# Kernel optimization log

Hardware: AMD Instinct MI355X
Metric: run time of the kernel (lower is better)

Reference implementation:

```python
import jax, jax.numpy as jnp
import numpy as np

TEMPERATURE = 0.1
WEIGHT = 0.1
EPS = 1e-12  # F.normalize clamp_min eps

B = 512   # number of reactions (batches)
G = 128   # atoms per reaction per side (uniform groups)
D = 256   # feature dim


def setup_inputs() -> dict:
    key = jax.random.key(0)
    k1, k2, k3, k4 = jax.random.split(key, 4)
    preds = jax.random.normal(k1, (B,), dtype=jnp.float32)
    y = jax.random.normal(k2, (B,), dtype=jnp.float32)
    reactant_features = jax.random.normal(k3, (B * G, D), dtype=jnp.float32)
    product_features = jax.random.normal(k4, (B * G, D), dtype=jnp.float32)
    # sorted, uniform-size groups: [0]*G, [1]*G, ...
    batch_idx = jnp.repeat(jnp.arange(B, dtype=jnp.int64), G)
    return {
        "preds": preds,
        "y": y,
        "reactant_features": reactant_features,
        "product_features": product_features,
        "reactant_batch_indices": batch_idx,
        "product_batch_indices": batch_idx,
    }


def _l2_normalize(x):
    # matches F.normalize(p=2, dim=1): x / max(||x||, eps)
    n = jnp.sqrt(jnp.sum(x * x, axis=-1, keepdims=True))
    return x / jnp.maximum(n, EPS)


def reference(preds, y, reactant_features, product_features,
              reactant_batch_indices, product_batch_indices):
    # MSE with reduction='sum'
    mse_loss = jnp.sum((preds - y) ** 2)

    # groups are uniform and sorted -> per-batch gather == reshape
    nb = int(reactant_batch_indices[-1]) + 1          # number of unique batches
    g = reactant_features.shape[0] // nb
    d = reactant_features.shape[1]
    r = reactant_features.reshape(nb, g, d)
    p = product_features.reshape(nb, g, d)

    rn = _l2_normalize(r)
    pn = _l2_normalize(p)
    # per-batch similarity [nb, g, g]
    sim = jnp.einsum('bgd,bhd->bgh', rn, pn) / TEMPERATURE

    # cross_entropy with labels = arange(g), mean over rows (torch default)
    lse = jax.scipy.special.logsumexp(sim, axis=-1)   # [nb, g]
    diag = jnp.einsum('bgg->bg', sim)                 # logits at true labels
    ce_per_batch = jnp.mean(lse - diag, axis=-1)      # [nb]
    contrastive_loss = jnp.mean(ce_per_batch)         # sum over batches / nb

    return mse_loss + WEIGHT * contrastive_loss
```

## Files before the change

kernel.cpp:

```cpp
#include <hip/hip_runtime.h>
#include <math.h>

#define BATCH 512
#define G 128
#define D 256
#define LRB 264

typedef __attribute__((ext_vector_type(8))) short short8;
typedef __attribute__((ext_vector_type(4))) float f32x4;
typedef __attribute__((ext_vector_type(4))) int  i32x4;

__device__ __forceinline__ unsigned int pack2bf16(float a, float b) {
    unsigned int ua = __float_as_uint(a);
    unsigned int ub = __float_as_uint(b);
    ua = (ua + 0x7FFFu + ((ua >> 16) & 1u)) >> 16;
    ub = (ub + 0x7FFFu + ((ub >> 16) & 1u)) >> 16;
    return ua | (ub << 16);
}

#define WAITVM(N)  asm volatile("s_waitcnt vmcnt(" #N ")" ::: "memory")
#define WAITLGKM0  asm volatile("s_waitcnt lgkmcnt(0)" ::: "memory")
#define FENCE      asm volatile("" ::: "memory")

__global__ __launch_bounds__(512, 4)
void fused_kernel(const float* __restrict__ rfeat,
                  const float* __restrict__ pfeat,
                  const float* __restrict__ preds,
                  const float* __restrict__ yv,
                  float* __restrict__ out)
{
    const int b = blockIdx.x;
    const float* rb = rfeat + (size_t)b * (G * D);
    const float* pb = pfeat + (size_t)b * (G * D);

    __shared__ unsigned short psh[G * LRB];
    __shared__ float inv_r[G];
    __shared__ float inv_p[G];
    __shared__ float red[8];

    const int tid  = threadIdx.x;
    const int lane = tid & 63;
    const int wv   = tid >> 6;
    const int lg   = lane >> 4;
    const int lc   = lane & 15;
    const int prow = tid >> 3;
    const int psl  = tid & 7;

    float pd = 0.f, yd = 0.f;
    if (b == 0) { pd = preds[tid]; yd = yv[tid]; }
    FENCE;

    float4 pv[8];
#pragma unroll
    for (int j = 0; j < 8; ++j)
        pv[j] = *reinterpret_cast<const float4*>(pb + prow * D + (psl + 8 * j) * 4);
    FENCE;

    const float* rptr = rb + (wv * 16 + lc) * D + lg * 8;
    float4 rx[16];
#pragma unroll
    for (int ks = 0; ks < 8; ++ks) {
        rx[2 * ks]     = *reinterpret_cast<const float4*>(rptr + ks * 32);
        rx[2 * ks + 1] = *reinterpret_cast<const float4*>(rptr + ks * 32 + 4);
    }
    FENCE;

    WAITVM(16);
    float contrib = 0.f;
    if (b == 0) { float dd = pd - yd; contrib = dd * dd; }
    {
        float ss = 0.f;
#pragma unroll
        for (int j = 0; j < 8; ++j) {
            const float4 v = pv[j];
            ss += v.x*v.x + v.y*v.y + v.z*v.z + v.w*v.w;
            *reinterpret_cast<uint2*>(&psh[prow * LRB + (psl + 8 * j) * 4]) =
                make_uint2(pack2bf16(v.x, v.y), pack2bf16(v.z, v.w));
        }
#pragma unroll
        for (int off = 1; off < 8; off <<= 1) ss += __shfl_xor(ss, off);
        if (psl == 0) inv_p[prow] = 1.0f / fmaxf(sqrtf(ss), 1e-12f);
    }
    FENCE;

#pragma unroll
    for (int j = 0; j < 8; ++j)
        pv[j] = *reinterpret_cast<const float4*>(pb + (64 + prow) * D + (psl + 8 * j) * 4);
    FENCE;

    WAITVM(8);
    short8 afr[8];
    float nrsum = 0.f;
#pragma unroll
    for (int ks = 0; ks < 8; ++ks) {
        const float4 x0 = rx[2 * ks], x1 = rx[2 * ks + 1];
        nrsum += x0.x*x0.x + x0.y*x0.y + x0.z*x0.z + x0.w*x0.w
               + x1.x*x1.x + x1.y*x1.y + x1.z*x1.z + x1.w*x1.w;
        i32x4 pk = { (int)pack2bf16(x0.x, x0.y), (int)pack2bf16(x0.z, x0.w),
                     (int)pack2bf16(x1.x, x1.y), (int)pack2bf16(x1.z, x1.w) };
        union { i32x4 i; short8 s; } u; u.i = pk;
        afr[ks] = u.s;
    }
    nrsum += __shfl_xor(nrsum, 16);
    nrsum += __shfl_xor(nrsum, 32);
    if (lane < 16)
        inv_r[wv * 16 + lane] = 10.0f / fmaxf(sqrtf(nrsum), 1e-12f);

    WAITLGKM0;
    __builtin_amdgcn_s_barrier();
    FENCE;

    f32x4 acc[8];
#pragma unroll
    for (int nj = 0; nj < 8; ++nj) acc[nj] = (f32x4){0.f, 0.f, 0.f, 0.f};

#pragma unroll
    for (int ks = 0; ks < 8; ++ks) {
        const int kb = ks * 32 + lg * 8;
#pragma unroll
        for (int nj = 0; nj < 4; ++nj) {
            short8 bf = *reinterpret_cast<const short8*>(&psh[(nj * 16 + lc) * LRB + kb]);
            acc[nj] = __builtin_amdgcn_mfma_f32_16x16x32_bf16(afr[ks], bf, acc[nj], 0, 0, 0);
        }
    }
    FENCE;

    WAITVM(0);
    {
        float ss = 0.f;
#pragma unroll
        for (int j = 0; j < 8; ++j) {
            const float4 v = pv[j];
            ss += v.x*v.x + v.y*v.y + v.z*v.z + v.w*v.w;
            *reinterpret_cast<uint2*>(&psh[(64 + prow) * LRB + (psl + 8 * j) * 4]) =
                make_uint2(pack2bf16(v.x, v.y), pack2bf16(v.z, v.w));
        }
#pragma unroll
        for (int off = 1; off < 8; off <<= 1) ss += __shfl_xor(ss, off);
        if (psl == 0) inv_p[64 + prow] = 1.0f / fmaxf(sqrtf(ss), 1e-12f);
    }

    WAITLGKM0;
    __builtin_amdgcn_s_barrier();
    FENCE;

#pragma unroll
    for (int ks = 0; ks < 8; ++ks) {
        const int kb = ks * 32 + lg * 8;
#pragma unroll
        for (int nj = 4; nj < 8; ++nj) {
            short8 bf = *reinterpret_cast<const short8*>(&psh[(nj * 16 + lc) * LRB + kb]);
            acc[nj] = __builtin_amdgcn_mfma_f32_16x16x32_bf16(afr[ks], bf, acc[nj], 0, 0, 0);
        }
    }

    float invp_r[8];
#pragma unroll
    for (int nj = 0; nj < 8; ++nj) invp_r[nj] = inv_p[nj * 16 + lc];

    const int njd = wv;
    float ce_part = 0.f;
#pragma unroll
    for (int reg = 0; reg < 4; ++reg) {
        const int rrow = lg * 4 + reg;
        const float invr_g = inv_r[wv * 16 + rrow];
        float s[8];
        float m = -3.0e38f;
#pragma unroll
        for (int nj = 0; nj < 8; ++nj) {
            s[nj] = acc[nj][reg] * invr_g * invp_r[nj];
            m = fmaxf(m, s[nj]);
        }
#pragma unroll
        for (int off = 1; off < 16; off <<= 1) m = fmaxf(m, __shfl_xor(m, off));
        float e = 0.f;
#pragma unroll
        for (int nj = 0; nj < 8; ++nj) e += __expf(s[nj] - m);
#pragma unroll
        for (int off = 1; off < 16; off <<= 1) e += __shfl_xor(e, off);
        if (lc == rrow)
            ce_part += (m + __logf(e)) - s[njd];
    }

    contrib += ce_part * (0.1f / ((float)BATCH * (float)G));
#pragma unroll
    for (int off = 1; off < 64; off <<= 1) contrib += __shfl_xor(contrib, off);
    if (lane == 0) red[wv] = contrib;
    __syncthreads();
    if (tid == 0) {
        float t = 0.f;
#pragma unroll
        for (int i = 0; i < 8; ++i) t += red[i];
        atomicAdd(out, t);
    }
}

extern "C" void kernel_launch(void* const* d_in, const int* in_sizes, int n_in,
                              void* d_out, int out_size, void* d_ws, size_t ws_size,
                              hipStream_t stream) {
    const float* preds = (const float*)d_in[0];
    const float* yv    = (const float*)d_in[1];
    const float* rf    = (const float*)d_in[2];
    const float* pf    = (const float*)d_in[3];
    float* out = (float*)d_out;
    (void)d_ws; (void)ws_size;

    hipMemsetAsync(out, 0, (size_t)out_size * sizeof(float), stream);
    fused_kernel<<<BATCH, 512, 0, stream>>>(rf, pf, preds, yv, out);
}
```

Before: 36.48 us.

## Split each batch across two blocks and stream products through double-buffered LDS

Each reaction batch is now handled by two 256-thread blocks, each owning 64 reactant rows, giving 1024 blocks. The product matrix is streamed in four 32-row quarters through a two-slot LDS double buffer, so loads overlap the packing and MFMA work and LDS per block shrinks. The cost is that every product row is loaded, normalised and packed twice, once per half-block, which doubles product-side global traffic. The per-block work is also split into more barrier-separated phases. A block-index swizzle pairs the two halves of a batch so they run close together and can share L2.

```diff
diff --git a/kernel.cpp b/kernel.cpp
--- a/kernel.cpp
+++ b/kernel.cpp
@@ -4,6 +4,7 @@
 #define BATCH 512
 #define G 128
 #define D 256
+#define QR 32
 #define LRB 264
 
 typedef __attribute__((ext_vector_type(8))) short short8;
@@ -22,21 +23,24 @@
 #define WAITLGKM0  asm volatile("s_waitcnt lgkmcnt(0)" ::: "memory")
 #define FENCE      asm volatile("" ::: "memory")
 
-__global__ __launch_bounds__(512, 4)
+__global__ __launch_bounds__(256, 4)
 void fused_kernel(const float* __restrict__ rfeat,
                   const float* __restrict__ pfeat,
                   const float* __restrict__ preds,
                   const float* __restrict__ yv,
                   float* __restrict__ out)
 {
-    const int b = blockIdx.x;
-    const float* rb = rfeat + (size_t)b * (G * D);
+    const int bid = blockIdx.x;
+    const int b = (bid & 7) | ((bid >> 4) << 3);
+    const int h = (bid >> 3) & 1;
+
+    const float* rb = rfeat + (size_t)b * (G * D) + (size_t)(h * 64) * D;
     const float* pb = pfeat + (size_t)b * (G * D);
 
-    __shared__ unsigned short psh[G * LRB];
-    __shared__ float inv_r[G];
+    __shared__ unsigned short psh[2][QR * LRB];
+    __shared__ float inv_r[64];
     __shared__ float inv_p[G];
-    __shared__ float red[8];
+    __shared__ float red[4];
 
     const int tid  = threadIdx.x;
     const int lane = tid & 63;
@@ -46,16 +50,38 @@
     const int prow = tid >> 3;
     const int psl  = tid & 7;
 
-    float pd = 0.f, yd = 0.f;
-    if (b == 0) { pd = preds[tid]; yd = yv[tid]; }
-    FENCE;
+#define ISSUEQ(q)                                                               \
+    _Pragma("unroll")                                                           \
+    for (int j = 0; j < 8; ++j)                                                 \
+        pv[j] = *reinterpret_cast<const float4*>(pb + ((q) * QR + prow) * D + (psl + 8 * j) * 4);
+
+#define PACKQ(q, buf) {                                                         \
+        float ss = 0.f;                                                         \
+        _Pragma("unroll")                                                       \
+        for (int j = 0; j < 8; ++j) {                                           \
+            const float4 v = pv[j];                                             \
+            ss += v.x*v.x + v.y*v.y + v.z*v.z + v.w*v.w;                        \
+            *reinterpret_cast<uint2*>(&psh[buf][prow * LRB + (psl + 8 * j) * 4]) \
+                = make_uint2(pack2bf16(v.x, v.y), pack2bf16(v.z, v.w));         \
+        }                                                                       \
+        _Pragma("unroll")                                                       \
+        for (int off = 1; off < 8; off <<= 1) ss += __shfl_xor(ss, off);        \
+        if (psl == 0) inv_p[(q) * QR + prow] = 1.0f / fmaxf(sqrtf(ss), 1e-12f); \
+    }
+
+#define MFMAQ(q, buf)                                                           \
+    _Pragma("unroll")                                                           \
+    for (int ks = 0; ks < 8; ++ks) {                                            \
+        const int kb = ks * 32 + lg * 8;                                        \
+        short8 b0 = *reinterpret_cast<const short8*>(&psh[buf][lc * LRB + kb]);        \
+        short8 b1 = *reinterpret_cast<const short8*>(&psh[buf][(16 + lc) * LRB + kb]); \
+        acc[2*(q)]   = __builtin_amdgcn_mfma_f32_16x16x32_bf16(afr[ks], b0, acc[2*(q)],   0, 0, 0); \
+        acc[2*(q)+1] = __builtin_amdgcn_mfma_f32_16x16x32_bf16(afr[ks], b1, acc[2*(q)+1], 0, 0, 0); \
+    }
 
     float4 pv[8];
-#pragma unroll
-    for (int j = 0; j < 8; ++j)
-        pv[j] = *reinterpret_cast<const float4*>(pb + prow * D + (psl + 8 * j) * 4);
-    FENCE;
-
+    ISSUEQ(0);
+    FENCE;
     const float* rptr = rb + (wv * 16 + lc) * D + lg * 8;
     float4 rx[16];
 #pragma unroll
@@ -66,26 +92,9 @@
     FENCE;
 
     WAITVM(16);
-    float contrib = 0.f;
-    if (b == 0) { float dd = pd - yd; contrib = dd * dd; }
-    {
-        float ss = 0.f;
-#pragma unroll
-        for (int j = 0; j < 8; ++j) {
-            const float4 v = pv[j];
-            ss += v.x*v.x + v.y*v.y + v.z*v.z + v.w*v.w;
-            *reinterpret_cast<uint2*>(&psh[prow * LRB + (psl + 8 * j) * 4]) =
-                make_uint2(pack2bf16(v.x, v.y), pack2bf16(v.z, v.w));
-        }
-#pragma unroll
-        for (int off = 1; off < 8; off <<= 1) ss += __shfl_xor(ss, off);
-        if (psl == 0) inv_p[prow] = 1.0f / fmaxf(sqrtf(ss), 1e-12f);
-    }
-    FENCE;
-
-#pragma unroll
-    for (int j = 0; j < 8; ++j)
-        pv[j] = *reinterpret_cast<const float4*>(pb + (64 + prow) * D + (psl + 8 * j) * 4);
+    PACKQ(0, 0);
+    FENCE;
+    ISSUEQ(1);
     FENCE;
 
     WAITVM(8);
@@ -106,59 +115,43 @@
     if (lane < 16)
         inv_r[wv * 16 + lane] = 10.0f / fmaxf(sqrtf(nrsum), 1e-12f);
 
-    WAITLGKM0;
-    __builtin_amdgcn_s_barrier();
-    FENCE;
-
     f32x4 acc[8];
 #pragma unroll
     for (int nj = 0; nj < 8; ++nj) acc[nj] = (f32x4){0.f, 0.f, 0.f, 0.f};
 
-#pragma unroll
-    for (int ks = 0; ks < 8; ++ks) {
-        const int kb = ks * 32 + lg * 8;
-#pragma unroll
-        for (int nj = 0; nj < 4; ++nj) {
-            short8 bf = *reinterpret_cast<const short8*>(&psh[(nj * 16 + lc) * LRB + kb]);
-            acc[nj] = __builtin_amdgcn_mfma_f32_16x16x32_bf16(afr[ks], bf, acc[nj], 0, 0, 0);
-        }
-    }
+    WAITLGKM0; __builtin_amdgcn_s_barrier(); FENCE;
+    MFMAQ(0, 0);
     FENCE;
 
     WAITVM(0);
-    {
-        float ss = 0.f;
-#pragma unroll
-        for (int j = 0; j < 8; ++j) {
-            const float4 v = pv[j];
-            ss += v.x*v.x + v.y*v.y + v.z*v.z + v.w*v.w;
-            *reinterpret_cast<uint2*>(&psh[(64 + prow) * LRB + (psl + 8 * j) * 4]) =
-                make_uint2(pack2bf16(v.x, v.y), pack2bf16(v.z, v.w));
-        }
-#pragma unroll
-        for (int off = 1; off < 8; off <<= 1) ss += __shfl_xor(ss, off);
-        if (psl == 0) inv_p[64 + prow] = 1.0f / fmaxf(sqrtf(ss), 1e-12f);
-    }
-
-    WAITLGKM0;
-    __builtin_amdgcn_s_barrier();
-    FENCE;
-
-#pragma unroll
-    for (int ks = 0; ks < 8; ++ks) {
-        const int kb = ks * 32 + lg * 8;
-#pragma unroll
-        for (int nj = 4; nj < 8; ++nj) {
-            short8 bf = *reinterpret_cast<const short8*>(&psh[(nj * 16 + lc) * LRB + kb]);
-            acc[nj] = __builtin_amdgcn_mfma_f32_16x16x32_bf16(afr[ks], bf, acc[nj], 0, 0, 0);
-        }
-    }
+    PACKQ(1, 1);
+    FENCE;
+    ISSUEQ(2);
+    FENCE;
+    WAITLGKM0; __builtin_amdgcn_s_barrier(); FENCE;
+    MFMAQ(1, 1);
+    FENCE;
+
+    WAITVM(0);
+    PACKQ(2, 0);
+    FENCE;
+    ISSUEQ(3);
+    FENCE;
+    WAITLGKM0; __builtin_amdgcn_s_barrier(); FENCE;
+    MFMAQ(2, 0);
+    FENCE;
+
+    WAITVM(0);
+    PACKQ(3, 1);
+    FENCE;
+    WAITLGKM0; __builtin_amdgcn_s_barrier(); FENCE;
+    MFMAQ(3, 1);
 
     float invp_r[8];
 #pragma unroll
     for (int nj = 0; nj < 8; ++nj) invp_r[nj] = inv_p[nj * 16 + lc];
 
-    const int njd = wv;
+    const int njd = 4 * h + wv;
     float ce_part = 0.f;
 #pragma unroll
     for (int reg = 0; reg < 4; ++reg) {
@@ -182,17 +175,22 @@
             ce_part += (m + __logf(e)) - s[njd];
     }
 
-    contrib += ce_part * (0.1f / ((float)BATCH * (float)G));
+    float contrib = ce_part * (0.1f / ((float)BATCH * (float)G));
+    if (b == 0 && h == 0) {
+        float d1 = preds[tid]       - yv[tid];
+        float d2 = preds[tid + 256] - yv[tid + 256];
+        contrib += d1 * d1 + d2 * d2;
+    }
 #pragma unroll
     for (int off = 1; off < 64; off <<= 1) contrib += __shfl_xor(contrib, off);
     if (lane == 0) red[wv] = contrib;
     __syncthreads();
-    if (tid == 0) {
-        float t = 0.f;
-#pragma unroll
-        for (int i = 0; i < 8; ++i) t += red[i];
-        atomicAdd(out, t);
-    }
+    if (tid == 0)
+        atomicAdd(out, red[0] + red[1] + red[2] + red[3]);
+
+#undef ISSUEQ
+#undef PACKQ
+#undef MFMAQ
 }
 
 extern "C" void kernel_launch(void* const* d_in, const int* in_sizes, int n_in,
@@ -206,5 +204,5 @@
     (void)d_ws; (void)ws_size;
 
     hipMemsetAsync(out, 0, (size_t)out_size * sizeof(float), stream);
-    fused_kernel<<<BATCH, 512, 0, stream>>>(rf, pf, preds, yv, out);
+    fused_kernel<<<2 * BATCH, 256, 0, stream>>>(rf, pf, preds, yv, out);
 }
```

Result: slower. 46.87 us (+28.5%).
